# Kernel optimization log

Hardware: AMD Instinct MI355X
Metric: run time of the kernel (lower is better)

The kernel has to match this reference:

```python
import jax, jax.numpy as jnp
import numpy as np


def setup_inputs() -> dict:
    key = jax.random.key(0)
    k1, k2, k3 = jax.random.split(key, 3)
    B, D, T = 16, 64, 8192
    n_codebook, n_emb = 4, 512
    z_e_x = jax.random.normal(k1, (B, D, T), dtype=jnp.float32)
    # torch init is uniform(-1/n_emb, 1/n_emb)
    codebook = jax.random.uniform(k2, (n_codebook, D, n_emb), dtype=jnp.float32,
                                  minval=-1.0 / n_emb, maxval=1.0 / n_emb)
    codebook_index = jax.random.randint(k3, (1,), 0, n_codebook, dtype=jnp.int64)
    return {"z_e_x": z_e_x, "codebook": codebook, "codebook_index": codebook_index}


def reference(z_e_x, codebook, codebook_index):
    # codebook: [n_codebook, D, n_emb]; select one codebook -> [D, n_emb]
    cb = codebook[codebook_index[0]]
    B, D, T = z_e_x.shape
    # [B, D, T] -> [B*T, D]
    z = jnp.transpose(z_e_x, (0, 2, 1)).reshape(-1, D)
    # squared L2 distances to each code: [B*T, n_emb]
    dist2 = (jnp.sum(z * z, axis=1, keepdims=True)
             - 2.0 * (z @ cb)
             + jnp.sum(cb * cb, axis=0))
    z_id_flat = jnp.argmax(-dist2, axis=1)          # nearest code index, [B*T]
    z_id = z_id_flat.reshape(B, T)
    z_q = cb.T[z_id_flat].reshape(B, T, D)          # gather codes
    z_q = jnp.transpose(z_q, (0, 2, 1))             # [B, D, T]
    return z_q, z_id
```

## Files before the change

### kernel.cpp

```cpp
#include <hip/hip_runtime.h>


constexpr int Dc = 64, Ec = 512, Tc = 8192;
constexpr int QTOT = 131072, ZQ = 8388608;
constexpr int QPB = 256;
constexpr int NBLK = QTOT / QPB;

using half8  = __attribute__((ext_vector_type(8))) _Float16;
using f32x16 = __attribute__((ext_vector_type(16))) float;

__global__ void vq_prep(const float* __restrict__ cbfull, const int* __restrict__ cbidx,
                        _Float16* __restrict__ wsf) {
    int tid = blockIdx.x * 256 + threadIdx.x;
    const float* cb = cbfull + (size_t)(cbidx[0] & 3) * (Dc * Ec);
    if (tid < 512) {
        float c = cb[tid];
        float a = __fmul_rn(c, c);
        for (int d = 1; d < Dc; ++d) { c = cb[d * Ec + tid]; a = __fadd_rn(a, __fmul_rn(c, c)); }
        ((float*)(wsf + 32768))[tid] = a;
    }
    if (tid >= 4096) return;
    int l = tid & 63, c = (tid >> 6) & 3, g = tid >> 8;
    int n = g * 32 + (l & 31);
    int kbase = c * 16 + (l >> 5) * 8;
    _Float16* dst = wsf + (size_t)(g * 4 + c) * 512 + l * 8;
    #pragma unroll
    for (int i = 0; i < 8; ++i)
        dst[i] = (_Float16)(cb[(kbase + i) * Ec + n] * 512.0f);
}

__global__ __launch_bounds__(512) void vq_main(
    const float* __restrict__ z, const float* __restrict__ cbfull,
    const int* __restrict__ cbidx, _Float16* __restrict__ wsf,
    float* __restrict__ out) {
    __shared__ __attribute__((aligned(16))) _Float16 s_frag[32768];
    __shared__ float s_c2[Ec];
    __shared__ unsigned s_w[QPB];
    __shared__ int s_idx[QPB];

    const int tid = threadIdx.x;
    const int lane = tid & 63;
    const int wave = __builtin_amdgcn_readfirstlane(tid >> 6);
    const int col = lane & 31, hh = lane >> 5;
    const int q0 = blockIdx.x * QPB;
    const int b = q0 >> 13, t0 = q0 & (Tc - 1);
    const int myq = wave * 32 + col;
    const int t = t0 + myq;

    const int ci = cbidx[0] & 3;
    const float* __restrict__ cb = cbfull + (size_t)ci * (Dc * Ec);

    float zv[32];
    const float* zp = z + (size_t)b * Dc * Tc + t;
    #pragma unroll
    for (int c = 0; c < 4; ++c)
        #pragma unroll
        for (int i = 0; i < 8; ++i)
            zv[c * 8 + i] = zp[(size_t)(c * 16 + hh * 8 + i) * Tc];

    {
        const uint4* src = (const uint4*)wsf;
        uint4* dst = (uint4*)s_frag;
        #pragma unroll
        for (int k = 0; k < 8; ++k) dst[tid + k * 512] = src[tid + k * 512];
    }
    if (tid < 512) s_c2[tid] = ((const float*)(wsf + 32768))[tid];

    float s1p = 0.f;
    #pragma unroll
    for (int e = 0; e < 32; ++e) s1p = __fmaf_rn(zv[e], zv[e], s1p);
    float s1b = (s1p + __shfl_xor(s1p, 32, 64)) * 1.001f + 0.01f;
    float wf = 2.5e-7f * (s1b + 1.f) + 3.2e-5f * sqrtf(s1b) + 1e-5f;
    unsigned w_int = (s1b > 880.f) ? 0x7FFFFFFFu : (unsigned)(wf * 2.147483648e9f) + 512u;
    if (hh == 0) s_w[myq] = w_int;

    half8 uhf[4], ulf[4];
    #pragma unroll
    for (int c = 0; c < 4; ++c)
        #pragma unroll
        for (int i = 0; i < 8; ++i) {
            float f = -16.0f * zv[c * 8 + i];
            _Float16 h = (_Float16)f;
            float hf = (float)h;
            uhf[c][i] = h;
            ulf[c][i] = (_Float16)(f - hf);
        }

    __syncthreads();

    unsigned m1[16], m2[16];
    #pragma unroll
    for (int r = 0; r < 16; ++r) { m1[r] = 0xFFFFFFFFu; m2[r] = 0xFFFFFFFFu; }

    #pragma unroll 2
    for (int g = 0; g < 16; ++g) {
        const float kb = __fmaf_rn(s_c2[g * 32 + col], 4096.0f, 12288.0f);
        f32x16 acc;
        #pragma unroll
        for (int r = 0; r < 16; ++r) acc[r] = kb;
        #pragma unroll
        for (int c = 0; c < 4; ++c) {
            half8 chf = *(const half8*)(s_frag + (size_t)(g * 4 + c) * 512 + lane * 8);
            acc = __builtin_amdgcn_mfma_f32_32x32x16_f16(uhf[c], chf, acc, 0, 0, 0);
            acc = __builtin_amdgcn_mfma_f32_32x32x16_f16(ulf[c], chf, acc, 0, 0, 0);
        }
        const unsigned jj = (unsigned)(g * 32 + col);
        #pragma unroll
        for (int r = 0; r < 16; ++r) {
            unsigned key = (__float_as_uint(acc[r]) << 9) | jj;
            unsigned mx = key > m1[r] ? key : m1[r];
            m1[r] = key < m1[r] ? key : m1[r];
            m2[r] = mx < m2[r] ? mx : m2[r];
        }
    }

    #pragma unroll
    for (int st = 1; st < 32; st <<= 1) {
        #pragma unroll
        for (int r = 0; r < 16; ++r) {
            unsigned o1 = __shfl_xor(m1[r], st, 64);
            unsigned o2 = __shfl_xor(m2[r], st, 64);
            unsigned mx = m1[r] > o1 ? m1[r] : o1;
            m1[r] = m1[r] < o1 ? m1[r] : o1;
            m2[r] = m2[r] < o2 ? m2[r] : o2;
            m2[r] = m2[r] < mx ? m2[r] : mx;
        }
    }

    unsigned F1 = 0xFFFFFFFFu, F2 = 0xFFFFFFFFu;
    #pragma unroll
    for (int r = 0; r < 16; ++r) if (col == r) { F1 = m1[r]; F2 = m2[r]; }
    bool amb = false;
    if (col < 16) {
        int row = (col & 3) + 8 * (col >> 2) + 4 * hh;
        int Q = wave * 32 + row;
        s_idx[Q] = (int)(F1 & 511u);
        unsigned wq = s_w[Q];
        amb = ((unsigned long long)F2 <= (unsigned long long)F1 + wq);
    }
    unsigned long long bal = __ballot(amb);
    if (lane == 0)
        ((unsigned long long*)(wsf + 33792))[blockIdx.x * 8 + wave] = bal;
    __syncthreads();

    #pragma unroll
    for (int qh = 0; qh < 4; ++qh) {
        const int ql = qh * 64 + lane;
        const int jj = s_idx[ql];
        const int tt = t0 + ql;
        float* op = out + ((size_t)b * Dc + wave * 8) * Tc + tt;
        #pragma unroll
        for (int dd = 0; dd < 8; ++dd)
            op[(size_t)dd * Tc] = cb[(wave * 8 + dd) * Ec + jj];
        if (wave == 0) out[ZQ + q0 + ql] = (float)jj;
    }
}

__global__ __launch_bounds__(64) void vq_rescan(
    const float* __restrict__ z, const float* __restrict__ cbfull,
    const int* __restrict__ cbidx, const _Float16* __restrict__ wsf,
    float* __restrict__ out) {
    const int lane = threadIdx.x;
    unsigned long long mask = ((const unsigned long long*)(wsf + 33792))[blockIdx.x];
    if (mask == 0) return;

    const int ci = cbidx[0] & 3;
    const float* __restrict__ cb = cbfull + (size_t)ci * (Dc * Ec);
    const float* __restrict__ c2g = (const float*)(wsf + 32768);
    const int qbase = (blockIdx.x >> 3) * QPB + (blockIdx.x & 7) * 32;
    const int b = qbase >> 13, tb = qbase & (Tc - 1);

    while (mask) {
        int L = __ffsll(mask) - 1; mask &= mask - 1;
        int r = L & 31, hb = L >> 5;
        int row = (r & 3) + 8 * (r >> 2) + 4 * hb;
        int q = qbase + row, t = tb + row;
        const float* zq = z + (size_t)b * Dc * Tc + t;
        float zr[64];
        #pragma unroll
        for (int d = 0; d < 64; ++d) zr[d] = zq[(size_t)d * Tc];
        float rr[8];
        #pragma unroll
        for (int u = 0; u < 8; ++u) rr[u] = __fmul_rn(zr[u], zr[u]);
        #pragma unroll
        for (int i = 8; i < 64; i += 8)
            #pragma unroll
            for (int u = 0; u < 8; ++u)
                rr[u] = __fadd_rn(rr[u], __fmul_rn(zr[i + u], zr[i + u]));
        float s1 = __fadd_rn(__fadd_rn(__fadd_rn(rr[0], rr[1]), __fadd_rn(rr[2], rr[3])),
                             __fadd_rn(__fadd_rn(rr[4], rr[5]), __fadd_rn(rr[6], rr[7])));
        float bk = __int_as_float(0x7f800000);
        int bj = 0;
        for (int u = 0; u < 8; ++u) {
            int j = u * 64 + lane;
            float G = 0.f;
            #pragma unroll
            for (int d = 0; d < 64; ++d) G = __fmaf_rn(zr[d], cb[d * Ec + j], G);
            float key = __fadd_rn(__fsub_rn(s1, __fmul_rn(2.0f, G)), c2g[j]);
            if (key < bk) { bk = key; bj = j; }
        }
        #pragma unroll
        for (int m = 1; m < 64; m <<= 1) {
            float pk = __shfl_xor(bk, m, 64);
            int pj = __shfl_xor(bj, m, 64);
            if (pk < bk || (pk == bk && pj < bj)) { bk = pk; bj = pj; }
        }
        out[((size_t)b * Dc + lane) * Tc + t] = cb[lane * Ec + bj];
        if (lane == 0) out[ZQ + q] = (float)bj;
    }
}

extern "C" void kernel_launch(void* const* d_in, const int* in_sizes, int n_in,
                              void* d_out, int out_size, void* d_ws, size_t ws_size,
                              hipStream_t stream) {
    const float* z = (const float*)d_in[0];
    const float* cbfull = (const float*)d_in[1];
    const int* cbidx = (const int*)d_in[2];
    _Float16* wsf = (_Float16*)d_ws;
    float* out = (float*)d_out;

    hipLaunchKernelGGL(vq_prep, dim3(16), dim3(256), 0, stream, cbfull, cbidx, wsf);
    hipLaunchKernelGGL(vq_main, dim3(NBLK), dim3(512), 0, stream, z, cbfull, cbidx, wsf, out);
    hipLaunchKernelGGL(vq_rescan, dim3(NBLK * 8), dim3(64), 0, stream, z, cbfull, cbidx, wsf, out);
}
```

Baseline: 113.6 us.

## Compact ambiguous queries into atomic worklist and rescan with persistent grid

Instead of writing one ballot mask per wave and launching 4096 single-wave rescan blocks that mostly exit immediately, the main kernel appends the ids of ambiguous queries to a global list through a per-wave atomicAdd. The rescan kernel is then launched as a fixed 256-block grid whose waves stride over the compacted list. This is meant to remove the launch and scheduling cost of thousands of empty blocks and to spread the real rescan work evenly across waves. It adds one global atomic per wave in the main kernel and a counter reset in the prep kernel. It also caps the list at 16384 entries, so any ambiguous queries beyond that cap would silently keep their approximate result.

```diff
diff --git a/kernel.cpp b/kernel.cpp
--- a/kernel.cpp
+++ b/kernel.cpp
@@ -5,13 +5,22 @@
 constexpr int QTOT = 131072, ZQ = 8388608;
 constexpr int QPB = 256;
 constexpr int NBLK = QTOT / QPB;
+constexpr int CAP = 16384;
 
 using half8  = __attribute__((ext_vector_type(8))) _Float16;
 using f32x16 = __attribute__((ext_vector_type(16))) float;
+
+__device__ __forceinline__ unsigned* ws_counter(_Float16* wsf) {
+    return (unsigned*)((char*)wsf + 67584);
+}
+__device__ __forceinline__ int* ws_list(_Float16* wsf) {
+    return (int*)((char*)wsf + 67600);
+}
 
 __global__ void vq_prep(const float* __restrict__ cbfull, const int* __restrict__ cbidx,
                         _Float16* __restrict__ wsf) {
     int tid = blockIdx.x * 256 + threadIdx.x;
+    if (tid == 0) *ws_counter(wsf) = 0;
     const float* cb = cbfull + (size_t)(cbidx[0] & 3) * (Dc * Ec);
     if (tid < 512) {
         float c = cb[tid];
@@ -131,16 +140,27 @@
     #pragma unroll
     for (int r = 0; r < 16; ++r) if (col == r) { F1 = m1[r]; F2 = m2[r]; }
     bool amb = false;
+    int Q = 0;
     if (col < 16) {
         int row = (col & 3) + 8 * (col >> 2) + 4 * hh;
-        int Q = wave * 32 + row;
+        Q = wave * 32 + row;
         s_idx[Q] = (int)(F1 & 511u);
         unsigned wq = s_w[Q];
         amb = ((unsigned long long)F2 <= (unsigned long long)F1 + wq);
     }
-    unsigned long long bal = __ballot(amb);
-    if (lane == 0)
-        ((unsigned long long*)(wsf + 33792))[blockIdx.x * 8 + wave] = bal;
+
+    {
+        unsigned long long bal = __ballot(amb);
+        int npop = __popcll(bal);
+        unsigned base = 0;
+        if (lane == 0 && npop) base = atomicAdd(ws_counter(wsf), (unsigned)npop);
+        base = __shfl(base, 0, 64);
+        if (amb) {
+            int rank = __popcll(bal & ((1ULL << lane) - 1ULL));
+            unsigned slot = base + (unsigned)rank;
+            if (slot < CAP) ws_list(wsf)[slot] = q0 + Q;
+        }
+    }
     __syncthreads();
 
     #pragma unroll
@@ -156,25 +176,25 @@
     }
 }
 
-__global__ __launch_bounds__(64) void vq_rescan(
+__global__ __launch_bounds__(256) void vq_rescan(
     const float* __restrict__ z, const float* __restrict__ cbfull,
-    const int* __restrict__ cbidx, const _Float16* __restrict__ wsf,
+    const int* __restrict__ cbidx, _Float16* __restrict__ wsf,
     float* __restrict__ out) {
-    const int lane = threadIdx.x;
-    unsigned long long mask = ((const unsigned long long*)(wsf + 33792))[blockIdx.x];
-    if (mask == 0) return;
+    const int lane = threadIdx.x & 63;
+    const int wv = threadIdx.x >> 6;
+    const unsigned cnt0 = *ws_counter(wsf);
+    const unsigned count = cnt0 < CAP ? cnt0 : CAP;
+    const int gw = blockIdx.x * 4 + wv;
+    if ((unsigned)gw >= count) return;
 
     const int ci = cbidx[0] & 3;
     const float* __restrict__ cb = cbfull + (size_t)ci * (Dc * Ec);
     const float* __restrict__ c2g = (const float*)(wsf + 32768);
-    const int qbase = (blockIdx.x >> 3) * QPB + (blockIdx.x & 7) * 32;
-    const int b = qbase >> 13, tb = qbase & (Tc - 1);
-
-    while (mask) {
-        int L = __ffsll(mask) - 1; mask &= mask - 1;
-        int r = L & 31, hb = L >> 5;
-        int row = (r & 3) + 8 * (r >> 2) + 4 * hb;
-        int q = qbase + row, t = tb + row;
+    const int* __restrict__ list = ws_list(wsf);
+
+    for (unsigned e = gw; e < count; e += 1024) {
+        const int qid = list[e];
+        const int b = qid >> 13, t = qid & (Tc - 1);
         const float* zq = z + (size_t)b * Dc * Tc + t;
         float zr[64];
         #pragma unroll
@@ -206,7 +226,7 @@
             if (pk < bk || (pk == bk && pj < bj)) { bk = pk; bj = pj; }
         }
         out[((size_t)b * Dc + lane) * Tc + t] = cb[lane * Ec + bj];
-        if (lane == 0) out[ZQ + q] = (float)bj;
+        if (lane == 0) out[ZQ + qid] = (float)bj;
     }
 }
 
@@ -221,5 +241,5 @@
 
     hipLaunchKernelGGL(vq_prep, dim3(16), dim3(256), 0, stream, cbfull, cbidx, wsf);
     hipLaunchKernelGGL(vq_main, dim3(NBLK), dim3(512), 0, stream, z, cbfull, cbidx, wsf, out);
-    hipLaunchKernelGGL(vq_rescan, dim3(NBLK * 8), dim3(64), 0, stream, z, cbfull, cbidx, wsf, out);
-}
+    hipLaunchKernelGGL(vq_rescan, dim3(256), dim3(256), 0, stream, z, cbfull, cbidx, wsf, out);
+}
```

Measured after the change: 405.7 us. +257.2%, slower.
